# Optimization experiments

Measured on AMD Instinct MI355X. Metric: run time of the kernel, lower is better.

## Reference

```python
import jax, jax.numpy as jnp
import numpy as np

B, S, D, E, K = 4, 4096, 4096, 64, 2
TEMP = 1.0  # temperature=1.0 -> scale by 1/temperature kept for faithfulness


def setup_inputs() -> dict:
    key = jax.random.key(0)
    k1, k2 = jax.random.split(key)
    x = jax.random.normal(k1, (B, S, D), dtype=jnp.float32)
    W_gate = jax.random.normal(k2, (E, D), dtype=jnp.float32) * (D ** -0.5)
    return {"x": x, "W_gate": W_gate}


def reference(x, W_gate):
    # gate: Linear(d_model, n_experts, bias=False) -> logits [B,S,E]
    logits = jnp.einsum('bsd,ed->bse', x, W_gate)
    # temperature scaling (eval mode: no jitter / expert dropout / gumbel)
    logits = logits * (1.0 / TEMP)
    probs_full = jax.nn.softmax(logits, axis=-1)           # [B,S,E]
    topk_vals, idx = jax.lax.top_k(logits, K)              # [B,S,K]
    scores = jax.nn.softmax(topk_vals, axis=-1)            # renormalized top-k gates
    # z-loss: mean(logsumexp(logits)^2)
    z = jax.nn.logsumexp(logits, axis=-1)                  # [B,S]
    z_loss = jnp.mean(z * z)
    # aux stats (computed under no_grad in the original)
    importance = jax.lax.stop_gradient(jnp.mean(probs_full, axis=(0, 1)))  # [E]
    idx_flat = idx.reshape(-1)
    counts = jnp.zeros((E,), probs_full.dtype).at[idx_flat].add(1.0)       # [E]
    load = jax.lax.stop_gradient(counts / jnp.maximum(jnp.sum(counts), 1.0))
    return (idx, scores, probs_full, z_loss, importance, load)
```

## Files before the change

kernel.cpp:

```cpp
#include <hip/hip_runtime.h>

namespace {
constexpr int D = 4096;
constexpr int E = 64;
constexpr int M = 16384;
constexpr int BM = 64;
constexpr int BK = 64;
constexpr int NT = D / BK;
constexpr int NBLK = M / BM;

constexpr int OFF_IDX = 0;
constexpr int OFF_SCORES = 32768;
constexpr int OFF_PROBS = 65536;
constexpr int OFF_Z = 1114112;
constexpr int OFF_IMP = 1114113;
constexpr int OFF_LOAD = 1114177;

constexpr int WS_STRIDE = 132;
}

__global__ __launch_bounds__(512, 2) void router_fused(
    const float* __restrict__ xg, const float* __restrict__ wg,
    float* __restrict__ out, float* __restrict__ ws) {
  __shared__ float smem[16384];

  const int t = threadIdx.x;
  const int u = t & 127;
  const int s = t >> 7;
  const int tx = u & 15;
  const int ty = u >> 4;
  const int r0 = blockIdx.x * BM;

  const int sr = t >> 3;
  const int sc = (t & 7) * 4;
  const float* xp = xg + (size_t)(r0 + sr) * D + sc;
  const float* wp = wg + (size_t)sr * D + sc;

  float4 vx[2], vw[2];

  auto stage_load = [&](int k0) {
    vx[0] = *(const float4*)(xp + k0);
    vx[1] = *(const float4*)(xp + k0 + 32);
    vw[0] = *(const float4*)(wp + k0);
    vw[1] = *(const float4*)(wp + k0 + 32);
  };
  auto stage_write = [&](float* buf) {
    float* Xs = buf;
    float* Ws = buf + 4096;
#pragma unroll
    for (int h = 0; h < 2; ++h) {
      const int c = sc + h * 32;
      const int sw = ((c >> 4) & 3) << 3;
      const int rp = sr ^ sw;
      Xs[(c + 0) * 64 + rp] = vx[h].x;
      Xs[(c + 1) * 64 + rp] = vx[h].y;
      Xs[(c + 2) * 64 + rp] = vx[h].z;
      Xs[(c + 3) * 64 + rp] = vx[h].w;
      Ws[(c + 0) * 64 + rp] = vw[h].x;
      Ws[(c + 1) * 64 + rp] = vw[h].y;
      Ws[(c + 2) * 64 + rp] = vw[h].z;
      Ws[(c + 3) * 64 + rp] = vw[h].w;
    }
  };

  float acc[8][4];
#pragma unroll
  for (int i = 0; i < 8; ++i)
#pragma unroll
    for (int j = 0; j < 4; ++j) acc[i][j] = 0.f;

  const int rbx = (ty * 8) ^ (s << 3);
  const int rbw = (tx * 4) ^ (s << 3);

  stage_load(0);
  stage_write(smem);

  for (int r = 0; r < NT; ++r) {
    __syncthreads();
    if (r + 1 < NT) stage_load((r + 1) * BK);

    const float* buf = smem + (r & 1) * 8192;
    const float* Xs = buf + (size_t)(s * 16) * 64;
    const float* Ws = buf + 4096 + (size_t)(s * 16) * 64;
#pragma unroll
    for (int kk = 0; kk < 16; ++kk) {
      const float4 a0 = *(const float4*)&Xs[kk * 64 + rbx];
      const float4 a1 = *(const float4*)&Xs[kk * 64 + rbx + 4];
      const float4 bw = *(const float4*)&Ws[kk * 64 + rbw];
      const float av[8] = {a0.x, a0.y, a0.z, a0.w, a1.x, a1.y, a1.z, a1.w};
      const float bv[4] = {bw.x, bw.y, bw.z, bw.w};
#pragma unroll
      for (int i = 0; i < 8; ++i)
#pragma unroll
        for (int j = 0; j < 4; ++j) acc[i][j] = fmaf(av[i], bv[j], acc[i][j]);
    }
    if (r + 1 < NT) stage_write(smem + ((r + 1) & 1) * 8192);
  }

  float* P = smem;
  __syncthreads();
  if (s >= 2) {
    float* p = P + ((size_t)((s - 2) * 128 + u)) * 33;
#pragma unroll
    for (int i = 0; i < 8; ++i)
#pragma unroll
      for (int j = 0; j < 4; ++j) p[i * 4 + j] = acc[i][j];
  }
  __syncthreads();
  if (s < 2) {
    const float* p = P + ((size_t)(s * 128 + u)) * 33;
#pragma unroll
    for (int i = 0; i < 8; ++i)
#pragma unroll
      for (int j = 0; j < 4; ++j) acc[i][j] += p[i * 4 + j];
  }
  __syncthreads();
  if (s == 1) {
    float* p = P + (size_t)u * 33;
#pragma unroll
    for (int i = 0; i < 8; ++i)
#pragma unroll
      for (int j = 0; j < 4; ++j) p[i * 4 + j] = acc[i][j];
  }
  __syncthreads();

  float* Lg = smem + 8448;
  float* rowmax = smem + 12608;
  float* rowrs = rowmax + 64;
  float* zrow = rowrs + 64;
  int* cnt = (int*)(zrow + 64);

  if (s == 0) {
    const float* p = P + (size_t)u * 33;
#pragma unroll
    for (int i = 0; i < 8; ++i)
#pragma unroll
      for (int j = 0; j < 4; ++j) {
        const float v = acc[i][j] + p[i * 4 + j];
        Lg[(ty * 8 + i) * 65 + tx * 4 + j] = v;
      }
  }
  if (t < 64) cnt[t] = 0;
  __syncthreads();

  if (t < 64) {
    const float* row = Lg + t * 65;
    float v1 = -3.402823466e+38f, v2 = -3.402823466e+38f;
    int i1 = 0, i2 = 0;
#pragma unroll 8
    for (int e = 0; e < 64; ++e) {
      const float x = row[e];
      if (x > v1) {
        v2 = v1; i2 = i1; v1 = x; i1 = e;
      } else if (x > v2) {
        v2 = x; i2 = e;
      }
    }
    float ssum = 0.f;
#pragma unroll 8
    for (int e = 0; e < 64; ++e) ssum += __expf(row[e] - v1);
    const float z = v1 + __logf(ssum);
    rowmax[t] = v1;
    rowrs[t] = 1.f / ssum;
    zrow[t] = z * z;

    const int r = r0 + t;
    out[OFF_IDX + 2 * r] = (float)i1;
    out[OFF_IDX + 2 * r + 1] = (float)i2;
    const float e1 = __expf(v2 - v1);
    const float s0 = 1.f / (1.f + e1);
    out[OFF_SCORES + 2 * r] = s0;
    out[OFF_SCORES + 2 * r + 1] = e1 * s0;
    atomicAdd(&cnt[i1], 1);
    atomicAdd(&cnt[i2], 1);
  }
  __syncthreads();

  {
    const int pr = t >> 3;
    const int pc = (t & 7) * 8;
    float* prow = Lg + pr * 65 + pc;
    const float m = rowmax[pr];
    const float rs = rowrs[pr];
    float p[8];
#pragma unroll
    for (int q = 0; q < 8; ++q) p[q] = __expf(prow[q] - m) * rs;
    float4 o0 = {p[0], p[1], p[2], p[3]};
    float4 o1 = {p[4], p[5], p[6], p[7]};
    *(float4*)&out[OFF_PROBS + (size_t)(r0 + pr) * 64 + pc] = o0;
    *(float4*)&out[OFF_PROBS + (size_t)(r0 + pr) * 64 + pc + 4] = o1;
#pragma unroll
    for (int q = 0; q < 8; ++q) prow[q] = p[q];
  }
  __syncthreads();

  if (t < 64) {
    float ic = 0.f;
#pragma unroll 8
    for (int rr = 0; rr < 64; ++rr) ic += Lg[rr * 65 + t];
    ws[(size_t)blockIdx.x * WS_STRIDE + t] = ic;
    ws[(size_t)blockIdx.x * WS_STRIDE + 64 + t] = (float)cnt[t];
    float zz = zrow[t];
#pragma unroll
    for (int off = 32; off > 0; off >>= 1) zz += __shfl_xor(zz, off);
    if (t == 0) ws[(size_t)blockIdx.x * WS_STRIDE + 128] = zz;
  }
}

__global__ __launch_bounds__(192) void router_reduce(
    const float* __restrict__ ws, float* __restrict__ out) {
  const int t = threadIdx.x;
  if (t < 129) {
    float v = 0.f;
#pragma unroll 8
    for (int b = 0; b < NBLK; ++b) v += ws[(size_t)b * WS_STRIDE + t];
    if (t < 64)
      out[OFF_IMP + t] = v * (1.f / 16384.f);
    else if (t < 128)
      out[OFF_LOAD + (t - 64)] = v * (1.f / 32768.f);
    else
      out[OFF_Z] = v * (1.f / 16384.f);
  }
}

extern "C" void kernel_launch(void* const* d_in, const int* in_sizes, int n_in,
                              void* d_out, int out_size, void* d_ws, size_t ws_size,
                              hipStream_t stream) {
  const float* x = (const float*)d_in[0];
  const float* wgate = (const float*)d_in[1];
  float* out = (float*)d_out;
  float* ws = (float*)d_ws;

  router_fused<<<dim3(NBLK), dim3(512), 0, stream>>>(x, wgate, out, ws);
  router_reduce<<<dim3(1), dim3(192), 0, stream>>>(ws, out);
}
```

Measured before the change: 409.0 us.

## Halve row tile to 32 and split K across 16 slices with tree reduction

Shrinks the per-block row tile from 64 to 32, doubling the grid to 512 blocks, and reorganizes the 512 threads into 16 K-slices of 32 threads, each computing an 8x8 register tile over a 4-wide K chunk. The old 4-way split-K merge is replaced by a 4-level shared-memory tree reduction, and the shared layout, swizzles and epilogue indexing are adjusted for 32 rows. Launch bounds now request 4 blocks per CU. The aim is more parallelism and occupancy for this bandwidth-bound skinny GEMM, at the cost of more reduction syncs, twice the W_gate reads overall, and 64 accumulators per thread under a tighter register cap.

```diff
diff --git a/kernel.cpp b/kernel.cpp
--- a/kernel.cpp
+++ b/kernel.cpp
@@ -4,7 +4,7 @@
 constexpr int D = 4096;
 constexpr int E = 64;
 constexpr int M = 16384;
-constexpr int BM = 64;
+constexpr int BM = 32;
 constexpr int BK = 64;
 constexpr int NT = D / BK;
 constexpr int NBLK = M / BM;
@@ -17,60 +17,67 @@
 constexpr int OFF_LOAD = 1114177;
 
 constexpr int WS_STRIDE = 132;
-}
-
-__global__ __launch_bounds__(512, 2) void router_fused(
+
+constexpr int WOFF = 2048;
+constexpr int BUFSZ = 6144;
+}
+
+__global__ __launch_bounds__(512, 4) void router_fused(
     const float* __restrict__ xg, const float* __restrict__ wg,
     float* __restrict__ out, float* __restrict__ ws) {
   __shared__ float smem[16384];
 
   const int t = threadIdx.x;
-  const int u = t & 127;
-  const int s = t >> 7;
-  const int tx = u & 15;
-  const int ty = u >> 4;
+  const int slice = t >> 5;
+  const int tile = t & 31;
+  const int rg = tile >> 3;
+  const int eg = tile & 7;
   const int r0 = blockIdx.x * BM;
 
-  const int sr = t >> 3;
-  const int sc = (t & 7) * 4;
-  const float* xp = xg + (size_t)(r0 + sr) * D + sc;
-  const float* wp = wg + (size_t)sr * D + sc;
-
-  float4 vx[2], vw[2];
-
+  const int srow = t >> 4;
+  const int skq = (t & 15) * 4;
+  const int ssw = (t & 7) << 2;
+  const float* xp = xg + (size_t)(r0 + srow) * D + skq;
+  const float* wp0 = wg + (size_t)srow * D + skq;
+  const float* wp1 = wg + (size_t)(srow + 32) * D + skq;
+
+  float4 vx, vw0, vw1;
   auto stage_load = [&](int k0) {
-    vx[0] = *(const float4*)(xp + k0);
-    vx[1] = *(const float4*)(xp + k0 + 32);
-    vw[0] = *(const float4*)(wp + k0);
-    vw[1] = *(const float4*)(wp + k0 + 32);
+    vx = *(const float4*)(xp + k0);
+    vw0 = *(const float4*)(wp0 + k0);
+    vw1 = *(const float4*)(wp1 + k0);
   };
   auto stage_write = [&](float* buf) {
     float* Xs = buf;
-    float* Ws = buf + 4096;
-#pragma unroll
-    for (int h = 0; h < 2; ++h) {
-      const int c = sc + h * 32;
-      const int sw = ((c >> 4) & 3) << 3;
-      const int rp = sr ^ sw;
-      Xs[(c + 0) * 64 + rp] = vx[h].x;
-      Xs[(c + 1) * 64 + rp] = vx[h].y;
-      Xs[(c + 2) * 64 + rp] = vx[h].z;
-      Xs[(c + 3) * 64 + rp] = vx[h].w;
-      Ws[(c + 0) * 64 + rp] = vw[h].x;
-      Ws[(c + 1) * 64 + rp] = vw[h].y;
-      Ws[(c + 2) * 64 + rp] = vw[h].z;
-      Ws[(c + 3) * 64 + rp] = vw[h].w;
-    }
+    float* Ws = buf + WOFF;
+    const int xr = srow ^ ssw;
+    const int w0 = srow ^ ssw;
+    const int w1 = (srow + 32) ^ ssw;
+    Xs[(skq + 0) * 32 + xr] = vx.x;
+    Xs[(skq + 1) * 32 + xr] = vx.y;
+    Xs[(skq + 2) * 32 + xr] = vx.z;
+    Xs[(skq + 3) * 32 + xr] = vx.w;
+    Ws[(skq + 0) * 64 + w0] = vw0.x;
+    Ws[(skq + 1) * 64 + w0] = vw0.y;
+    Ws[(skq + 2) * 64 + w0] = vw0.z;
+    Ws[(skq + 3) * 64 + w0] = vw0.w;
+    Ws[(skq + 0) * 64 + w1] = vw1.x;
+    Ws[(skq + 1) * 64 + w1] = vw1.y;
+    Ws[(skq + 2) * 64 + w1] = vw1.z;
+    Ws[(skq + 3) * 64 + w1] = vw1.w;
   };
 
-  float acc[8][4];
+  const int sxr = (slice & 7) << 2;
+  const int xb0 = (rg * 8) ^ sxr;
+  const int xb1 = (rg * 8 + 4) ^ sxr;
+  const int wb0 = (eg * 8) ^ sxr;
+  const int wb1 = (eg * 8 + 4) ^ sxr;
+
+  float acc[8][8];
 #pragma unroll
   for (int i = 0; i < 8; ++i)
 #pragma unroll
-    for (int j = 0; j < 4; ++j) acc[i][j] = 0.f;
-
-  const int rbx = (ty * 8) ^ (s << 3);
-  const int rbw = (tx * 4) ^ (s << 3);
+    for (int j = 0; j < 8; ++j) acc[i][j] = 0.f;
 
   stage_load(0);
   stage_write(smem);
@@ -79,72 +86,77 @@
     __syncthreads();
     if (r + 1 < NT) stage_load((r + 1) * BK);
 
-    const float* buf = smem + (r & 1) * 8192;
-    const float* Xs = buf + (size_t)(s * 16) * 64;
-    const float* Ws = buf + 4096 + (size_t)(s * 16) * 64;
-#pragma unroll
-    for (int kk = 0; kk < 16; ++kk) {
-      const float4 a0 = *(const float4*)&Xs[kk * 64 + rbx];
-      const float4 a1 = *(const float4*)&Xs[kk * 64 + rbx + 4];
-      const float4 bw = *(const float4*)&Ws[kk * 64 + rbw];
+    const float* buf = smem + (r & 1) * BUFSZ;
+    const float* Xs = buf + slice * 4 * 32;
+    const float* Ws = buf + WOFF + slice * 4 * 64;
+#pragma unroll
+    for (int kk = 0; kk < 4; ++kk) {
+      const float4 a0 = *(const float4*)&Xs[kk * 32 + xb0];
+      const float4 a1 = *(const float4*)&Xs[kk * 32 + xb1];
+      const float4 b0 = *(const float4*)&Ws[kk * 64 + wb0];
+      const float4 b1 = *(const float4*)&Ws[kk * 64 + wb1];
       const float av[8] = {a0.x, a0.y, a0.z, a0.w, a1.x, a1.y, a1.z, a1.w};
-      const float bv[4] = {bw.x, bw.y, bw.z, bw.w};
+      const float bv[8] = {b0.x, b0.y, b0.z, b0.w, b1.x, b1.y, b1.z, b1.w};
 #pragma unroll
       for (int i = 0; i < 8; ++i)
 #pragma unroll
-        for (int j = 0; j < 4; ++j) acc[i][j] = fmaf(av[i], bv[j], acc[i][j]);
-    }
-    if (r + 1 < NT) stage_write(smem + ((r + 1) & 1) * 8192);
-  }
-
-  float* P = smem;
-  __syncthreads();
-  if (s >= 2) {
-    float* p = P + ((size_t)((s - 2) * 128 + u)) * 33;
+        for (int j = 0; j < 8; ++j) acc[i][j] = fmaf(av[i], bv[j], acc[i][j]);
+    }
+    if (r + 1 < NT) stage_write(smem + ((r + 1) & 1) * BUFSZ);
+  }
+  __syncthreads();
+
+#pragma unroll
+  for (int half = 8; half >= 1; half >>= 1) {
+    if (slice >= half && slice < 2 * half) {
+      float* p = smem + (size_t)((slice - half) * 32 + tile) * 64;
+#pragma unroll
+      for (int i = 0; i < 8; ++i)
+#pragma unroll
+        for (int j4 = 0; j4 < 8; j4 += 4) {
+          const int off = (i * 8 + j4 + tile * 4) & 63;
+          float4 v = {acc[i][j4], acc[i][j4 + 1], acc[i][j4 + 2], acc[i][j4 + 3]};
+          *(float4*)&p[off] = v;
+        }
+    }
+    __syncthreads();
+    if (slice < half) {
+      const float* p = smem + (size_t)(slice * 32 + tile) * 64;
+#pragma unroll
+      for (int i = 0; i < 8; ++i)
+#pragma unroll
+        for (int j4 = 0; j4 < 8; j4 += 4) {
+          const int off = (i * 8 + j4 + tile * 4) & 63;
+          const float4 v = *(const float4*)&p[off];
+          acc[i][j4] += v.x;
+          acc[i][j4 + 1] += v.y;
+          acc[i][j4 + 2] += v.z;
+          acc[i][j4 + 3] += v.w;
+        }
+    }
+    __syncthreads();
+  }
+
+  float* Lg = smem;
+  float* rowmax = smem + 2176;
+  float* rowrs = rowmax + 32;
+  float* zrow = rowrs + 32;
+  int* cnt = (int*)(zrow + 32);
+
+  if (slice == 0) {
 #pragma unroll
     for (int i = 0; i < 8; ++i)
 #pragma unroll
-      for (int j = 0; j < 4; ++j) p[i * 4 + j] = acc[i][j];
-  }
-  __syncthreads();
-  if (s < 2) {
-    const float* p = P + ((size_t)(s * 128 + u)) * 33;
-#pragma unroll
-    for (int i = 0; i < 8; ++i)
-#pragma unroll
-      for (int j = 0; j < 4; ++j) acc[i][j] += p[i * 4 + j];
-  }
-  __syncthreads();
-  if (s == 1) {
-    float* p = P + (size_t)u * 33;
-#pragma unroll
-    for (int i = 0; i < 8; ++i)
-#pragma unroll
-      for (int j = 0; j < 4; ++j) p[i * 4 + j] = acc[i][j];
-  }
-  __syncthreads();
-
-  float* Lg = smem + 8448;
-  float* rowmax = smem + 12608;
-  float* rowrs = rowmax + 64;
-  float* zrow = rowrs + 64;
-  int* cnt = (int*)(zrow + 64);
-
-  if (s == 0) {
-    const float* p = P + (size_t)u * 33;
-#pragma unroll
-    for (int i = 0; i < 8; ++i)
-#pragma unroll
-      for (int j = 0; j < 4; ++j) {
-        const float v = acc[i][j] + p[i * 4 + j];
-        Lg[(ty * 8 + i) * 65 + tx * 4 + j] = v;
+      for (int j4 = 0; j4 < 8; j4 += 4) {
+        float4 v = {acc[i][j4], acc[i][j4 + 1], acc[i][j4 + 2], acc[i][j4 + 3]};
+        *(float4*)&Lg[(rg * 8 + i) * 68 + eg * 8 + j4] = v;
       }
   }
   if (t < 64) cnt[t] = 0;
   __syncthreads();
 
-  if (t < 64) {
-    const float* row = Lg + t * 65;
+  if (t < 32) {
+    const float* row = Lg + t * 68;
     float v1 = -3.402823466e+38f, v2 = -3.402823466e+38f;
     int i1 = 0, i2 = 0;
 #pragma unroll 8
@@ -177,32 +189,32 @@
   __syncthreads();
 
   {
-    const int pr = t >> 3;
-    const int pc = (t & 7) * 8;
-    float* prow = Lg + pr * 65 + pc;
+    const int pr = t >> 4;
+    const int pc = (t & 15) * 4;
+    float* prow = Lg + pr * 68 + pc;
     const float m = rowmax[pr];
     const float rs = rowrs[pr];
-    float p[8];
-#pragma unroll
-    for (int q = 0; q < 8; ++q) p[q] = __expf(prow[q] - m) * rs;
-    float4 o0 = {p[0], p[1], p[2], p[3]};
-    float4 o1 = {p[4], p[5], p[6], p[7]};
-    *(float4*)&out[OFF_PROBS + (size_t)(r0 + pr) * 64 + pc] = o0;
-    *(float4*)&out[OFF_PROBS + (size_t)(r0 + pr) * 64 + pc + 4] = o1;
-#pragma unroll
-    for (int q = 0; q < 8; ++q) prow[q] = p[q];
+    float4 v = *(const float4*)prow;
+    v.x = __expf(v.x - m) * rs;
+    v.y = __expf(v.y - m) * rs;
+    v.z = __expf(v.z - m) * rs;
+    v.w = __expf(v.w - m) * rs;
+    *(float4*)&out[OFF_PROBS + (size_t)(r0 + pr) * 64 + pc] = v;
+    *(float4*)prow = v;
   }
   __syncthreads();
 
   if (t < 64) {
     float ic = 0.f;
 #pragma unroll 8
-    for (int rr = 0; rr < 64; ++rr) ic += Lg[rr * 65 + t];
+    for (int rr = 0; rr < 32; ++rr) ic += Lg[rr * 68 + t];
     ws[(size_t)blockIdx.x * WS_STRIDE + t] = ic;
     ws[(size_t)blockIdx.x * WS_STRIDE + 64 + t] = (float)cnt[t];
+  }
+  if (t < 32) {
     float zz = zrow[t];
 #pragma unroll
-    for (int off = 32; off > 0; off >>= 1) zz += __shfl_xor(zz, off);
+    for (int off = 16; off > 0; off >>= 1) zz += __shfl_xor(zz, off);
     if (t == 0) ws[(size_t)blockIdx.x * WS_STRIDE + 128] = zz;
   }
 }
```

After: 415.0 us. No clear change (+1.5%).
